# Performance work log

Hardware: AMD Instinct MI355X
Metric: run time of the kernel (lower is better)

Reference implementation:

```python
import jax, jax.numpy as jnp
import numpy as np

C = 1.0
TAU = 1.0
LE = 1.0
LH = 1.0
LN_EPS = 1e-5

def _safe_norm(x, keepdims=False):
    return jnp.clip(jnp.sqrt(jnp.sum(x * x, axis=-1, keepdims=keepdims)), 1e-15)

def _project_to_ball(x, c, eps=1e-5):
    sqrt_c = c ** 0.5
    norm = _safe_norm(x, keepdims=True)
    max_norm = (1.0 - eps) / sqrt_c
    scale = jnp.where(norm > max_norm, max_norm / norm, 1.0)
    return x * scale

def _lambda_x(x, c):
    x = _project_to_ball(x, c)
    x2 = jnp.sum(x * x, axis=-1, keepdims=True)
    return 2.0 / jnp.clip(1.0 - c * x2, 1e-15)

def _mobius_add(x, y, c):
    x = _project_to_ball(x, c)
    y = _project_to_ball(y, c)
    x2 = jnp.sum(x * x, axis=-1, keepdims=True)
    y2 = jnp.sum(y * y, axis=-1, keepdims=True)
    xy = jnp.sum(x * y, axis=-1, keepdims=True)
    num = (1 + 2 * c * xy + c * y2) * x + (1 - c * x2) * y
    den = 1 + 2 * c * xy + c ** 2 * x2 * y2
    return num / jnp.clip(den, 1e-15)

def _exp_map_x(x, v, c):
    sqrt_c = c ** 0.5
    lam = _lambda_x(x, c)
    vnorm = _safe_norm(v, keepdims=True)
    v_dir = v / vnorm
    factor = jnp.tanh(lam * sqrt_c * vnorm / 2.0) / sqrt_c
    out = _mobius_add(x, v_dir * factor, c)
    return _project_to_ball(out, c)

def _log_map_x(x, y, c):
    sqrt_c = c ** 0.5
    lam = _lambda_x(x, c)
    u = _mobius_add(-x, y, c)
    unorm = _safe_norm(u, keepdims=True)
    u_dir = u / unorm
    arg = jnp.minimum(sqrt_c * unorm, 1 - 1e-7)
    scale = 2.0 / (lam * sqrt_c) * jnp.arctanh(arg)
    return scale * u_dir

def _poincare_distance_sq(x, y, c):
    sqrt_c = c ** 0.5
    x = _project_to_ball(x, c)
    y = _project_to_ball(y, c)
    diff = _mobius_add(-x, y, c)
    norm = _safe_norm(diff, keepdims=False)
    arg = jnp.minimum(sqrt_c * norm, 1 - 1e-7)
    dist = 2.0 / sqrt_c * jnp.arctanh(arg)
    return dist * dist

def setup_inputs() -> dict:
    key = jax.random.key(0)
    ks = jax.random.split(key, 6)
    B, N, L, A, de, dh, z_dim = 8, 8, 64, 64, 128, 64, 128
    z_e, z_h = z_dim // 2 + z_dim % 2, z_dim // 2
    return {
        "curr_rho_batch": jax.random.normal(ks[0], (B, A, de), jnp.float32),
        "curr_hyp_emb": 0.1 * jax.random.normal(ks[1], (B, dh), jnp.float32),
        "demo_rho_batch": jax.random.normal(ks[2], (B, N, L, A, de), jnp.float32),
        "demo_hyp_emb": 0.1 * jax.random.normal(ks[3], (B, N, L, dh), jnp.float32),
        "We": 0.02 * jax.random.normal(ks[4], (z_e, de), jnp.float32),
        "Wh": 0.02 * jax.random.normal(ks[5], (z_h, dh), jnp.float32),
        "ln_gamma": jnp.ones((z_dim,), jnp.float32),
        "ln_beta": jnp.zeros((z_dim,), jnp.float32),
    }

def reference(curr_rho_batch, curr_hyp_emb, demo_rho_batch, demo_hyp_emb, We, Wh, ln_gamma, ln_beta):
    B, A, de = curr_rho_batch.shape
    _, N, L, _, _ = demo_rho_batch.shape
    M = N * L
    dh = curr_hyp_emb.shape[-1]
    demo_rho_flat = demo_rho_batch.reshape(B, M, A, de)   # [B,M,A,de]
    demo_hyp_flat = demo_hyp_emb.reshape(B, M, dh)        # [B,M,dh]
    # Euclidean squared distances: [B,M,A] -> [B,A,M]
    e_diff_sq = jnp.sum((curr_rho_batch[:, None, :, :] - demo_rho_flat) ** 2, axis=-1)
    e_diff_sq = jnp.transpose(e_diff_sq, (0, 2, 1))
    # Hyperbolic squared distances: [B,M]
    dH2 = _poincare_distance_sq(curr_hyp_emb[:, None, :], demo_hyp_flat, C)
    scores = -(LH * dH2[:, None, :] + LE * e_diff_sq) / max(TAU, 1e-8)  # [B,A,M]
    alpha = jax.nn.softmax(scores, axis=-1)
    # Euclidean aggregation
    e_out = jnp.einsum('bam,bmad->bad', alpha, demo_rho_flat)  # [B,A,de]
    # Hyperbolic Karcher-mean step
    log_vecs = _log_map_x(curr_hyp_emb[:, None, :], demo_hyp_flat, C)  # [B,M,dh]
    v = jnp.einsum('bam,bmd->bad', alpha, log_vecs)  # [B,A,dh]
    x_ba = jnp.broadcast_to(curr_hyp_emb[:, None, :], (B, A, dh))
    h_out = _exp_map_x(x_ba, v, C)  # [B,A,dh]
    z = jnp.concatenate([e_out @ We.T, h_out @ Wh.T], axis=-1)  # [B,A,z_dim]
    mean = jnp.mean(z, axis=-1, keepdims=True)
    var = jnp.var(z, axis=-1, keepdims=True)
    z = (z - mean) / jnp.sqrt(var + LN_EPS) * ln_gamma + ln_beta
    return z
```

## Files before the change

kernel.cpp:

```cpp
#include <hip/hip_runtime.h>

#define DEV __device__ __forceinline__

constexpr int A_ = 64, DE = 128, M_ = 512, DH = 64;

DEV float wred_sum64(float v) {
#pragma unroll
    for (int o = 1; o < 64; o <<= 1) v += __shfl_xor(v, o, 64);
    return v;
}

__global__ __launch_bounds__(256) void k_hyp(const float* __restrict__ curr_hyp,
                                             const float* __restrict__ demo_hyp,
                                             float* __restrict__ dH2,
                                             float* __restrict__ logv) {
    const int lane = threadIdx.x & 63;
    const int r    = (blockIdx.x << 2) + (threadIdx.x >> 6);
    const int b    = r >> 9;

    float x = curr_hyp[(b << 6) + lane];
    float y = demo_hyp[((size_t)r << 6) + lane];
    const float mx = 1.0f - 1e-5f;

    float x2r = wred_sum64(x * x);
    float xn  = fmaxf(sqrtf(x2r), 1e-15f);
    float sx  = xn > mx ? mx / xn : 1.0f;
    x *= sx;
    float x2 = x2r * sx * sx;
    float y2r = wred_sum64(y * y);
    float yn  = fmaxf(sqrtf(y2r), 1e-15f);
    float sy  = yn > mx ? mx / yn : 1.0f;
    y *= sy;
    float y2 = y2r * sy * sy;

    float xy = wred_sum64(x * y);
    float num = (1.f - 2.f * xy + y2) * (-x) + (1.f - x2) * y;
    float den = fmaxf(1.f - 2.f * xy + x2 * y2, 1e-15f);
    float u   = num / den;

    float u2  = wred_sum64(u * u);
    float un  = fmaxf(sqrtf(u2), 1e-15f);
    float arg = fminf(un, 1.f - 1e-7f);
    float at  = 0.5f * __logf((1.f + arg) / (1.f - arg));

    if (lane == 0) dH2[r] = 4.f * at * at;

    float lamden = fmaxf(1.f - x2, 1e-15f);
    float ls     = lamden * at / un;
    logv[((size_t)r << 6) + lane] = ls * u;
}

__global__ __launch_bounds__(512, 4) void k_stream2(const float* __restrict__ curr_rho,
                                                    const float* __restrict__ demo_rho,
                                                    const float* __restrict__ dH2,
                                                    float* __restrict__ ws_m,
                                                    float* __restrict__ ws_s,
                                                    float* __restrict__ ws_e,
                                                    float* __restrict__ ws_sc) {
    __shared__ float lds_dh[128];
    __shared__ float redm[8][4];
    __shared__ float reds[8][4];
    __shared__ __align__(16) float rede[8][512];

    const int t  = threadIdx.x;
    const int l  = t & 63;
    const int mi = t >> 6;
    const int al = l >> 4;
    const int dp = l & 15;
    const int blk = blockIdx.x;
    const int b  = blk >> 6;
    const int rr = blk & 63;
    const int mq = rr >> 4;
    const int aq = rr & 15;
    const int a  = aq * 4 + al;
    const int m0 = mq << 7;

    if (t < 128) lds_dh[t] = dH2[(b << 9) + m0 + t];

    float qf[8];
    {
        const float* qp = curr_rho + ((size_t)(b * 64 + a)) * DE + dp * 8;
        float4 q0 = *(const float4*)qp;
        float4 q1 = *(const float4*)(qp + 4);
        qf[0] = q0.x; qf[1] = q0.y; qf[2] = q0.z; qf[3] = q0.w;
        qf[4] = q1.x; qf[5] = q1.y; qf[6] = q1.z; qf[7] = q1.w;
    }

    const float* tp = demo_rho + ((size_t)(b * M_ + m0)) * (A_ * DE)
                    + (size_t)mi * 8192 + aq * 4 * DE + al * DE + dp * 8;
    const size_t CS = 65536;

    __syncthreads();

    float4 pa0 = *(const float4*)tp;
    float4 pa1 = *(const float4*)(tp + 4);
    float4 pb0 = *(const float4*)(tp + CS);
    float4 pb1 = *(const float4*)(tp + CS + 4);
    float4 pc0 = *(const float4*)(tp + 2 * CS);
    float4 pc1 = *(const float4*)(tp + 2 * CS + 4);

    float e_acc[8];
#pragma unroll
    for (int j = 0; j < 8; j++) e_acc[j] = 0.f;
    float gmax = -1e30f, gsum = 0.f;

#pragma unroll 4
    for (int c = 0; c < 16; ++c) {
        float4 n0 = make_float4(0.f, 0.f, 0.f, 0.f);
        float4 n1 = n0;
        if (c + 3 < 16) {
            const float* np = tp + (size_t)(c + 3) * CS;
            n0 = *(const float4*)np;
            n1 = *(const float4*)(np + 4);
        }
        float kf[8];
        kf[0] = pa0.x; kf[1] = pa0.y; kf[2] = pa0.z; kf[3] = pa0.w;
        kf[4] = pa1.x; kf[5] = pa1.y; kf[6] = pa1.z; kf[7] = pa1.w;

        float ps = 0.f;
#pragma unroll
        for (int j = 0; j < 8; j++) { float d = qf[j] - kf[j]; ps += d * d; }
        ps += __shfl_xor(ps, 1, 64);
        ps += __shfl_xor(ps, 2, 64);
        ps += __shfl_xor(ps, 4, 64);
        ps += __shfl_xor(ps, 8, 64);

        float sc = -(lds_dh[c * 8 + mi] + ps);
        if (dp == 0)
            ws_sc[((size_t)(b * M_ + m0 + c * 8 + mi)) * 64 + a] = sc;

        float gnew = fmaxf(gmax, sc);
        float r1   = __expf(gmax - gnew);
        float w    = __expf(sc - gnew);
        gsum = fmaf(gsum, r1, w);
#pragma unroll
        for (int j = 0; j < 8; j++) e_acc[j] = fmaf(w, kf[j], e_acc[j] * r1);
        gmax = gnew;

        pa0 = pb0; pa1 = pb1; pb0 = pc0; pb1 = pc1; pc0 = n0; pc1 = n1;
    }

    if (dp == 0) { redm[mi][al] = gmax; reds[mi][al] = gsum; }
    __syncthreads();

    float Mb = redm[0][al];
#pragma unroll
    for (int k = 1; k < 8; k++) Mb = fmaxf(Mb, redm[k][al]);
    float Sb = 0.f;
#pragma unroll
    for (int k = 0; k < 8; k++) Sb += reds[k][al] * __expf(redm[k][al] - Mb);
    float fac = __expf(gmax - Mb);

    *(float4*)&rede[mi][al * 128 + dp * 8] =
        make_float4(e_acc[0] * fac, e_acc[1] * fac, e_acc[2] * fac, e_acc[3] * fac);
    *(float4*)&rede[mi][al * 128 + dp * 8 + 4] =
        make_float4(e_acc[4] * fac, e_acc[5] * fac, e_acc[6] * fac, e_acc[7] * fac);
    if (mi == 0 && dp == 0) {
        const int q = b * 4 + mq;
        ws_m[q * 64 + a] = Mb;
        ws_s[q * 64 + a] = Sb;
    }
    __syncthreads();

    {
        const int al2 = t >> 7, dd = t & 127;
        float s = 0.f;
#pragma unroll
        for (int k = 0; k < 8; k++) s += rede[k][al2 * 128 + dd];
        ws_e[((size_t)(b * 4 + mq) * 64 + (aq * 4 + al2)) * 128 + dd] = s;
    }
}

__global__ __launch_bounds__(256) void k_comb2(const float* __restrict__ curr_hyp,
                                               const float* __restrict__ logv,
                                               const float* __restrict__ ws_m,
                                               const float* __restrict__ ws_s,
                                               const float* __restrict__ ws_e,
                                               const float* __restrict__ ws_sc,
                                               const float* __restrict__ We,
                                               const float* __restrict__ Wh,
                                               const float* __restrict__ gamma,
                                               const float* __restrict__ beta,
                                               float* __restrict__ out) {
    __shared__ float ehL[192];
    __shared__ float vpart[4][64];

    const int t   = threadIdx.x;
    const int blk = blockIdx.x;
    const int b   = blk >> 6, a = blk & 63;

    float m_[4], s_[4];
#pragma unroll
    for (int q = 0; q < 4; q++) {
        m_[q] = ws_m[(b * 4 + q) * 64 + a];
        s_[q] = ws_s[(b * 4 + q) * 64 + a];
    }
    float M = fmaxf(fmaxf(m_[0], m_[1]), fmaxf(m_[2], m_[3]));
    float S = 0.f;
#pragma unroll
    for (int q = 0; q < 4; q++) S += s_[q] * __expf(m_[q] - M);
    const float invS = 1.f / S;

    if (t < 128) {
        float acc = 0.f;
#pragma unroll
        for (int q = 0; q < 4; q++)
            acc = fmaf(ws_e[((size_t)(b * 4 + q) * 64 + a) * 128 + t], __expf(m_[q] - M), acc);
        ehL[t] = acc * invS;
    }

    {
        const int dh = t & 63, sg = t >> 6;
        const float* lvb = logv  + ((size_t)(b * M_ + sg * 128)) * 64 + dh;
        const float* scb = ws_sc + ((size_t)(b * M_ + sg * 128)) * 64 + a;
        float vac = 0.f;
#pragma unroll 8
        for (int i = 0; i < 128; ++i) {
            float w = __expf(scb[(size_t)i * 64] - M);
            vac = fmaf(w, lvb[(size_t)i * 64], vac);
        }
        vpart[sg][dh] = vac;
    }
    __syncthreads();

    if (t < 64) {
        const int lane = t;
        float v = (vpart[0][lane] + vpart[1][lane] + vpart[2][lane] + vpart[3][lane]) * invS;

        const float mx = 1.0f - 1e-5f;
        float x = curr_hyp[(b << 6) + lane];
        float x2r = wred_sum64(x * x);
        float xn  = fmaxf(sqrtf(x2r), 1e-15f);
        float sx  = xn > mx ? mx / xn : 1.f;
        x *= sx;
        float x2 = x2r * sx * sx;
        float lamden = fmaxf(1.f - x2, 1e-15f);

        float v2 = wred_sum64(v * v);
        float vn = fmaxf(sqrtf(v2), 1e-15f);
        float targ   = vn / lamden;
        float e2     = __expf(2.f * targ);
        float factor = 1.f - 2.f / (e2 + 1.f);
        float wvv    = v * (factor / vn);

        float w2 = wred_sum64(wvv * wvv);
        float xw = wred_sum64(x * wvv);
        float num = (1.f + 2.f * xw + w2) * x + (1.f - x2) * wvv;
        float den = fmaxf(1.f + 2.f * xw + x2 * w2, 1e-15f);
        float h   = num / den;
        float h2  = wred_sum64(h * h);
        float hn  = fmaxf(sqrtf(h2), 1e-15f);
        float shh = hn > mx ? mx / hn : 1.f;
        h *= shh;
        ehL[128 + lane] = h;

        float ze = 0.f;
        const float* werow = We + lane * 128;
#pragma unroll
        for (int d0 = 0; d0 < 128; d0 += 4) {
            float4 wv4 = *(const float4*)(werow + d0);
            ze = fmaf(ehL[d0 + 0], wv4.x, ze);
            ze = fmaf(ehL[d0 + 1], wv4.y, ze);
            ze = fmaf(ehL[d0 + 2], wv4.z, ze);
            ze = fmaf(ehL[d0 + 3], wv4.w, ze);
        }
        float zh = 0.f;
        const float* whrow = Wh + lane * 64;
#pragma unroll
        for (int d0 = 0; d0 < 64; d0 += 4) {
            float4 wv4 = *(const float4*)(whrow + d0);
            zh = fmaf(ehL[128 + d0 + 0], wv4.x, zh);
            zh = fmaf(ehL[128 + d0 + 1], wv4.y, zh);
            zh = fmaf(ehL[128 + d0 + 2], wv4.z, zh);
            zh = fmaf(ehL[128 + d0 + 3], wv4.w, zh);
        }
        float ssum = wred_sum64(ze + zh);
        float mean = ssum * (1.f / 128.f);
        float sq   = wred_sum64(ze * ze + zh * zh);
        float var  = sq * (1.f / 128.f) - mean * mean;
        float rinv = rsqrtf(var + 1e-5f);
        float oe = (ze - mean) * rinv * gamma[lane] + beta[lane];
        float oh = (zh - mean) * rinv * gamma[64 + lane] + beta[64 + lane];
        out[(size_t)blk * 128 + lane]      = oe;
        out[(size_t)blk * 128 + 64 + lane] = oh;
    }
}

extern "C" void kernel_launch(void* const* d_in, const int* in_sizes, int n_in,
                              void* d_out, int out_size, void* d_ws, size_t ws_size,
                              hipStream_t stream) {
    const float* curr_rho = (const float*)d_in[0];
    const float* curr_hyp = (const float*)d_in[1];
    const float* demo_rho = (const float*)d_in[2];
    const float* demo_hyp = (const float*)d_in[3];
    const float* We       = (const float*)d_in[4];
    const float* Wh       = (const float*)d_in[5];
    const float* gamma    = (const float*)d_in[6];
    const float* beta     = (const float*)d_in[7];
    float* out = (float*)d_out;

    float* ws    = (float*)d_ws;
    float* dH2   = ws;
    float* logv  = ws + 4096;
    float* ws_m  = ws + 266240;
    float* ws_s  = ws + 268288;
    float* ws_e  = ws + 270336;
    float* ws_sc = ws + 532480;

    k_hyp<<<1024, 256, 0, stream>>>(curr_hyp, demo_hyp, dH2, logv);
    k_stream2<<<512, 512, 0, stream>>>(curr_rho, demo_rho, dH2, ws_m, ws_s, ws_e, ws_sc);
    k_comb2<<<512, 256, 0, stream>>>(curr_hyp, logv, ws_m, ws_s, ws_e, ws_sc,
                                     We, Wh, gamma, beta, out);
}
```

Measured before the change: 221.6 us.

## Split M into 32 chunks per block and defer softmax merge to combine kernel

The streaming kernel now assigns one block per (batch, 16-demo chunk) with 1024 threads covering all 64 agents. Each thread writes its partial max, sum and weighted sum straight to workspace, which removes the LDS cross-wave reduction and its barriers. The combine kernel merges 32 partials per row with wave shuffles, and precomputes the exp weights into LDS from a transposed, contiguous score layout. The grid drops to 256 blocks of 1024 threads, and the partial-sum workspace grows eightfold, adding extra write and read traffic.

```diff
diff --git a/kernel.cpp b/kernel.cpp
--- a/kernel.cpp
+++ b/kernel.cpp
@@ -50,66 +50,60 @@
     logv[((size_t)r << 6) + lane] = ls * u;
 }
 
-__global__ __launch_bounds__(512, 4) void k_stream2(const float* __restrict__ curr_rho,
-                                                    const float* __restrict__ demo_rho,
-                                                    const float* __restrict__ dH2,
-                                                    float* __restrict__ ws_m,
-                                                    float* __restrict__ ws_s,
-                                                    float* __restrict__ ws_e,
-                                                    float* __restrict__ ws_sc) {
-    __shared__ float lds_dh[128];
-    __shared__ float redm[8][4];
-    __shared__ float reds[8][4];
-    __shared__ __align__(16) float rede[8][512];
-
-    const int t  = threadIdx.x;
-    const int l  = t & 63;
-    const int mi = t >> 6;
-    const int al = l >> 4;
-    const int dp = l & 15;
+__global__ __launch_bounds__(1024) void k_stream3(const float* __restrict__ curr_rho,
+                                                  const float* __restrict__ demo_rho,
+                                                  const float* __restrict__ dH2,
+                                                  float* __restrict__ ws_m,
+                                                  float* __restrict__ ws_s,
+                                                  float* __restrict__ ws_e,
+                                                  float* __restrict__ ws_sc) {
+    const int t   = threadIdx.x;
+    const int mi  = t >> 4;
+    const int dp  = t & 15;
     const int blk = blockIdx.x;
-    const int b  = blk >> 6;
-    const int rr = blk & 63;
-    const int mq = rr >> 4;
-    const int aq = rr & 15;
-    const int a  = aq * 4 + al;
-    const int m0 = mq << 7;
-
-    if (t < 128) lds_dh[t] = dH2[(b << 9) + m0 + t];
+    const int b   = blk >> 5, mc = blk & 31;
+    const int m0  = mc << 4;
 
     float qf[8];
     {
-        const float* qp = curr_rho + ((size_t)(b * 64 + a)) * DE + dp * 8;
+        const float* qp = curr_rho + ((size_t)(b * 64 + mi)) * DE + dp * 8;
         float4 q0 = *(const float4*)qp;
         float4 q1 = *(const float4*)(qp + 4);
         qf[0] = q0.x; qf[1] = q0.y; qf[2] = q0.z; qf[3] = q0.w;
         qf[4] = q1.x; qf[5] = q1.y; qf[6] = q1.z; qf[7] = q1.w;
     }
 
-    const float* tp = demo_rho + ((size_t)(b * M_ + m0)) * (A_ * DE)
-                    + (size_t)mi * 8192 + aq * 4 * DE + al * DE + dp * 8;
-    const size_t CS = 65536;
-
-    __syncthreads();
+    float dh2r[16];
+    {
+        const float* dp2 = dH2 + (b << 9) + m0;
+        *(float4*)&dh2r[0]  = *(const float4*)(dp2);
+        *(float4*)&dh2r[4]  = *(const float4*)(dp2 + 4);
+        *(float4*)&dh2r[8]  = *(const float4*)(dp2 + 8);
+        *(float4*)&dh2r[12] = *(const float4*)(dp2 + 12);
+    }
+
+    const float* tp = demo_rho + ((size_t)(b * M_ + m0)) * (A_ * DE) + mi * DE + dp * 8;
 
     float4 pa0 = *(const float4*)tp;
     float4 pa1 = *(const float4*)(tp + 4);
-    float4 pb0 = *(const float4*)(tp + CS);
-    float4 pb1 = *(const float4*)(tp + CS + 4);
-    float4 pc0 = *(const float4*)(tp + 2 * CS);
-    float4 pc1 = *(const float4*)(tp + 2 * CS + 4);
+    float4 pb0 = *(const float4*)(tp + 8192);
+    float4 pb1 = *(const float4*)(tp + 8192 + 4);
+    float4 pc0 = *(const float4*)(tp + 16384);
+    float4 pc1 = *(const float4*)(tp + 16384 + 4);
 
     float e_acc[8];
 #pragma unroll
     for (int j = 0; j < 8; j++) e_acc[j] = 0.f;
     float gmax = -1e30f, gsum = 0.f;
 
-#pragma unroll 4
+    float* scp = ws_sc + ((size_t)(b * 64 + mi)) * 512 + m0;
+
+#pragma unroll
     for (int c = 0; c < 16; ++c) {
         float4 n0 = make_float4(0.f, 0.f, 0.f, 0.f);
         float4 n1 = n0;
         if (c + 3 < 16) {
-            const float* np = tp + (size_t)(c + 3) * CS;
+            const float* np = tp + (size_t)(c + 3) * 8192;
             n0 = *(const float4*)np;
             n1 = *(const float4*)(np + 4);
         }
@@ -125,9 +119,8 @@
         ps += __shfl_xor(ps, 4, 64);
         ps += __shfl_xor(ps, 8, 64);
 
-        float sc = -(lds_dh[c * 8 + mi] + ps);
-        if (dp == 0)
-            ws_sc[((size_t)(b * M_ + m0 + c * 8 + mi)) * 64 + a] = sc;
+        float sc = -(dh2r[c] + ps);
+        if (dp == 0) scp[c] = sc;
 
         float gnew = fmaxf(gmax, sc);
         float r1   = __expf(gmax - gnew);
@@ -140,38 +133,16 @@
         pa0 = pb0; pa1 = pb1; pb0 = pc0; pb1 = pc1; pc0 = n0; pc1 = n1;
     }
 
-    if (dp == 0) { redm[mi][al] = gmax; reds[mi][al] = gsum; }
-    __syncthreads();
-
-    float Mb = redm[0][al];
-#pragma unroll
-    for (int k = 1; k < 8; k++) Mb = fmaxf(Mb, redm[k][al]);
-    float Sb = 0.f;
-#pragma unroll
-    for (int k = 0; k < 8; k++) Sb += reds[k][al] * __expf(redm[k][al] - Mb);
-    float fac = __expf(gmax - Mb);
-
-    *(float4*)&rede[mi][al * 128 + dp * 8] =
-        make_float4(e_acc[0] * fac, e_acc[1] * fac, e_acc[2] * fac, e_acc[3] * fac);
-    *(float4*)&rede[mi][al * 128 + dp * 8 + 4] =
-        make_float4(e_acc[4] * fac, e_acc[5] * fac, e_acc[6] * fac, e_acc[7] * fac);
-    if (mi == 0 && dp == 0) {
-        const int q = b * 4 + mq;
-        ws_m[q * 64 + a] = Mb;
-        ws_s[q * 64 + a] = Sb;
-    }
-    __syncthreads();
-
-    {
-        const int al2 = t >> 7, dd = t & 127;
-        float s = 0.f;
-#pragma unroll
-        for (int k = 0; k < 8; k++) s += rede[k][al2 * 128 + dd];
-        ws_e[((size_t)(b * 4 + mq) * 64 + (aq * 4 + al2)) * 128 + dd] = s;
-    }
-}
-
-__global__ __launch_bounds__(256) void k_comb2(const float* __restrict__ curr_hyp,
+    float* ep = ws_e + (((size_t)(b * 64 + mi)) * 32 + mc) * 128 + dp * 8;
+    *(float4*)ep       = make_float4(e_acc[0], e_acc[1], e_acc[2], e_acc[3]);
+    *(float4*)(ep + 4) = make_float4(e_acc[4], e_acc[5], e_acc[6], e_acc[7]);
+    if (dp == 0) {
+        ws_m[(b * 64 + mi) * 32 + mc] = gmax;
+        ws_s[(b * 64 + mi) * 32 + mc] = gsum;
+    }
+}
+
+__global__ __launch_bounds__(256) void k_comb3(const float* __restrict__ curr_hyp,
                                                const float* __restrict__ logv,
                                                const float* __restrict__ ws_m,
                                                const float* __restrict__ ws_s,
@@ -182,43 +153,64 @@
                                                const float* __restrict__ gamma,
                                                const float* __restrict__ beta,
                                                float* __restrict__ out) {
+    __shared__ float facL[32];
+    __shared__ float sMS[2];
+    __shared__ float wL[512];
     __shared__ float ehL[192];
     __shared__ float vpart[4][64];
 
     const int t   = threadIdx.x;
     const int blk = blockIdx.x;
     const int b   = blk >> 6, a = blk & 63;
-
-    float m_[4], s_[4];
-#pragma unroll
-    for (int q = 0; q < 4; q++) {
-        m_[q] = ws_m[(b * 4 + q) * 64 + a];
-        s_[q] = ws_s[(b * 4 + q) * 64 + a];
-    }
-    float M = fmaxf(fmaxf(m_[0], m_[1]), fmaxf(m_[2], m_[3]));
-    float S = 0.f;
-#pragma unroll
-    for (int q = 0; q < 4; q++) S += s_[q] * __expf(m_[q] - M);
-    const float invS = 1.f / S;
+    const size_t ba = (size_t)(b * 64 + a);
+
+    float g = -1e30f, s = 0.f;
+    if (t < 32) {
+        g = ws_m[ba * 32 + t];
+        s = ws_s[ba * 32 + t];
+    }
+    float M = g;
+    M = fmaxf(M, __shfl_xor(M, 1, 64));
+    M = fmaxf(M, __shfl_xor(M, 2, 64));
+    M = fmaxf(M, __shfl_xor(M, 4, 64));
+    M = fmaxf(M, __shfl_xor(M, 8, 64));
+    M = fmaxf(M, __shfl_xor(M, 16, 64));
+    float fac = __expf(g - M);
+    float Sp  = s * fac;
+    Sp += __shfl_xor(Sp, 1, 64);
+    Sp += __shfl_xor(Sp, 2, 64);
+    Sp += __shfl_xor(Sp, 4, 64);
+    Sp += __shfl_xor(Sp, 8, 64);
+    Sp += __shfl_xor(Sp, 16, 64);
+    if (t < 32) facL[t] = fac;
+    if (t == 0) { sMS[0] = M; sMS[1] = Sp; }
+    __syncthreads();
+    const float Mg   = sMS[0];
+    const float invS = 1.f / sMS[1];
 
     if (t < 128) {
+        const float* eb = ws_e + ba * (32 * 128) + t;
         float acc = 0.f;
 #pragma unroll
-        for (int q = 0; q < 4; q++)
-            acc = fmaf(ws_e[((size_t)(b * 4 + q) * 64 + a) * 128 + t], __expf(m_[q] - M), acc);
+        for (int mc = 0; mc < 32; ++mc)
+            acc = fmaf(eb[mc * 128], facL[mc], acc);
         ehL[t] = acc * invS;
     }
+
+    {
+        float2 scv = ((const float2*)(ws_sc + ba * 512))[t];
+        wL[2 * t]     = __expf(scv.x - Mg);
+        wL[2 * t + 1] = __expf(scv.y - Mg);
+    }
+    __syncthreads();
 
     {
         const int dh = t & 63, sg = t >> 6;
-        const float* lvb = logv  + ((size_t)(b * M_ + sg * 128)) * 64 + dh;
-        const float* scb = ws_sc + ((size_t)(b * M_ + sg * 128)) * 64 + a;
+        const float* lvb = logv + ((size_t)(b * M_ + sg * 128)) * 64 + dh;
         float vac = 0.f;
 #pragma unroll 8
-        for (int i = 0; i < 128; ++i) {
-            float w = __expf(scb[(size_t)i * 64] - M);
-            vac = fmaf(w, lvb[(size_t)i * 64], vac);
-        }
+        for (int i = 0; i < 128; ++i)
+            vac = fmaf(wL[sg * 128 + i], lvb[(size_t)i * 64], vac);
         vpart[sg][dh] = vac;
     }
     __syncthreads();
@@ -303,12 +295,12 @@
     float* dH2   = ws;
     float* logv  = ws + 4096;
     float* ws_m  = ws + 266240;
-    float* ws_s  = ws + 268288;
-    float* ws_e  = ws + 270336;
-    float* ws_sc = ws + 532480;
+    float* ws_s  = ws + 282624;
+    float* ws_e  = ws + 299008;
+    float* ws_sc = ws + 2396160;
 
     k_hyp<<<1024, 256, 0, stream>>>(curr_hyp, demo_hyp, dH2, logv);
-    k_stream2<<<512, 512, 0, stream>>>(curr_rho, demo_rho, dH2, ws_m, ws_s, ws_e, ws_sc);
-    k_comb2<<<512, 256, 0, stream>>>(curr_hyp, logv, ws_m, ws_s, ws_e, ws_sc,
+    k_stream3<<<256, 1024, 0, stream>>>(curr_rho, demo_rho, dH2, ws_m, ws_s, ws_e, ws_sc);
+    k_comb3<<<512, 256, 0, stream>>>(curr_hyp, logv, ws_m, ws_s, ws_e, ws_sc,
                                      We, Wh, gamma, beta, out);
 }
```

Measured after the change: 241.8 us. 9.1% more time.
